# Optimization experiments

Hardware: AMD Instinct MI355X
Metric: run time of the kernel (lower is better)

The kernel has to match this reference:

```python
import jax, jax.numpy as jnp
import numpy as np

N, F = 12288, 512
NEG_INF = jnp.float32(-1e9)  # matches Keras BaseDenseAttention mask additive constant


def setup_inputs() -> dict:
    key = jax.random.key(0)
    k1, k2 = jax.random.split(key)
    features = jax.random.normal(k1, (N, F), dtype=jnp.float32)
    A = jax.random.randint(k2, (N, N), 0, 2).astype(jnp.int32)
    return {"features": features, "A": A}


def reference(features, A):
    # Keras Attention with query=key=value=dropout(features); dropout is identity
    # at inference. use_scale=False -> plain dot-product scores, no 1/sqrt(d).
    scores = jnp.einsum("nf,mf->nm", features, features)          # [N, N]
    scores = jnp.where(A > 0, scores, NEG_INF)                    # mask non-edges
    attn = jax.nn.softmax(scores, axis=-1)                        # softmax over keys
    return jnp.einsum("nm,mf->nf", attn, features)                # [N, F]
```

## Files before the change

kernel.cpp:

```cpp
#include <hip/hip_runtime.h>
#include <cstddef>
#include <cstdint>

#define NN 12288
#define FF 512

using half8 = __attribute__((ext_vector_type(8))) _Float16;
using half4 = __attribute__((ext_vector_type(4))) _Float16;
using f32x4 = __attribute__((ext_vector_type(4))) float;

constexpr float MASK_NEG = -1e9f;

__device__ __forceinline__ void gll16(const void* g, void* l) {
    __builtin_amdgcn_global_load_lds((const __attribute__((address_space(1))) void*)g,
                                     (__attribute__((address_space(3))) void*)l, 16, 0, 0);
}

__global__ void cvt_feat_kernel(const float* __restrict__ in, _Float16* __restrict__ out) {
    const size_t i = ((size_t)blockIdx.x * blockDim.x + threadIdx.x) * 8;
    float4 x = *reinterpret_cast<const float4*>(in + i);
    float4 y = *reinterpret_cast<const float4*>(in + i + 4);
    half8 h;
    h[0] = (_Float16)x.x; h[1] = (_Float16)x.y; h[2] = (_Float16)x.z; h[3] = (_Float16)x.w;
    h[4] = (_Float16)y.x; h[5] = (_Float16)y.y; h[6] = (_Float16)y.z; h[7] = (_Float16)y.w;
    *reinterpret_cast<half8*>(out + i) = h;
}

__global__ void transpose_feat_kernel(const float* __restrict__ in, _Float16* __restrict__ outT) {
    __shared__ float tile[32][33];
    const int bi = blockIdx.x;
    const int bj = blockIdx.y;
    const int r  = threadIdx.x >> 3;
    const int c4 = (threadIdx.x & 7) << 2;
    float4 v = *reinterpret_cast<const float4*>(in + (size_t)(bi * 32 + r) * FF + bj * 32 + c4);
    tile[r][c4 + 0] = v.x; tile[r][c4 + 1] = v.y; tile[r][c4 + 2] = v.z; tile[r][c4 + 3] = v.w;
    __syncthreads();
    half4 h;
#pragma unroll
    for (int k = 0; k < 4; ++k) h[k] = (_Float16)tile[c4 + k][r];
    *reinterpret_cast<half4*>(outT + (size_t)(bj * 32 + r) * NN + bi * 32 + c4) = h;
}

__global__ __launch_bounds__(256)
void gemm1_exp(const _Float16* __restrict__ feath, const int* __restrict__ Amat,
               _Float16* __restrict__ Pmat, float* __restrict__ m_t) {
    __shared__ alignas(16) _Float16 As[2][128 * 32];
    __shared__ alignas(16) _Float16 Bs[2][128 * 32];
    __shared__ alignas(16) float rowmax2[128][2];

    const int tid = threadIdx.x, lane = tid & 63, wid = tid >> 6;
    const int g = lane >> 4, a = lane & 15;
    const int wr = wid >> 1, wc = wid & 1;
    const int row0 = blockIdx.x * 128, col0 = blockIdx.y * 128;

    f32x4 acc[4][4];
#pragma unroll
    for (int i = 0; i < 4; ++i)
#pragma unroll
        for (int j = 0; j < 4; ++j) acc[i][j] = f32x4{0.f, 0.f, 0.f, 0.f};

    const int lr = lane >> 2;
    const int li = (lane & 3) * 8;

    auto stage = [&](int buf, int t) {
#pragma unroll
        for (int c = 0; c < 2; ++c) {
            const int ch = wid * 2 + c;
            gll16(feath + (size_t)(row0 + ch * 16 + lr) * FF + t * 32 + li, &As[buf][ch * 512]);
            gll16(feath + (size_t)(col0 + ch * 16 + lr) * FF + t * 32 + li, &Bs[buf][ch * 512]);
        }
    };

    stage(0, 0);
    __syncthreads();
    int buf = 0;
    for (int t = 0; t < 16; ++t) {
        if (t + 1 < 16) stage(buf ^ 1, t + 1);
        half8 af[4], bf[4];
#pragma unroll
        for (int rf = 0; rf < 4; ++rf)
            af[rf] = *reinterpret_cast<const half8*>(&As[buf][(64 * wr + 16 * rf + a) * 32 + 8 * g]);
#pragma unroll
        for (int cf = 0; cf < 4; ++cf)
            bf[cf] = *reinterpret_cast<const half8*>(&Bs[buf][(64 * wc + 16 * cf + a) * 32 + 8 * g]);
#pragma unroll
        for (int rf = 0; rf < 4; ++rf)
#pragma unroll
            for (int cf = 0; cf < 4; ++cf)
                acc[rf][cf] = __builtin_amdgcn_mfma_f32_16x16x32_f16(af[rf], bf[cf], acc[rf][cf], 0, 0, 0);
        __syncthreads();
        buf ^= 1;
    }

#pragma unroll
    for (int rf = 0; rf < 4; ++rf) {
#pragma unroll
        for (int r = 0; r < 4; ++r) {
            const int grow = row0 + 64 * wr + 16 * rf + 4 * g + r;
#pragma unroll
            for (int cf = 0; cf < 4; ++cf) {
                const int gcol = col0 + 64 * wc + 16 * cf + a;
                const int am = Amat[(size_t)grow * NN + gcol];
                acc[rf][cf][r] = (am > 0) ? acc[rf][cf][r] : MASK_NEG;
            }
        }
    }
#pragma unroll
    for (int rf = 0; rf < 4; ++rf) {
#pragma unroll
        for (int r = 0; r < 4; ++r) {
            float v = fmaxf(fmaxf(acc[rf][0][r], acc[rf][1][r]), fmaxf(acc[rf][2][r], acc[rf][3][r]));
            v = fmaxf(v, __shfl_xor(v, 1, 16));
            v = fmaxf(v, __shfl_xor(v, 2, 16));
            v = fmaxf(v, __shfl_xor(v, 4, 16));
            v = fmaxf(v, __shfl_xor(v, 8, 16));
            if (a == 0) rowmax2[64 * wr + 16 * rf + 4 * g + r][wc] = v;
        }
    }
    __syncthreads();
    if (tid < 128)
        m_t[(size_t)blockIdx.y * NN + row0 + tid] = fmaxf(rowmax2[tid][0], rowmax2[tid][1]);
#pragma unroll
    for (int rf = 0; rf < 4; ++rf) {
#pragma unroll
        for (int r = 0; r < 4; ++r) {
            const int lrow = 64 * wr + 16 * rf + 4 * g + r;
            const float mt = fmaxf(rowmax2[lrow][0], rowmax2[lrow][1]);
            const size_t rbase = (size_t)(row0 + lrow) * NN + col0 + 64 * wc + a;
#pragma unroll
            for (int cf = 0; cf < 4; ++cf) {
                const float p = __expf(acc[rf][cf][r] - mt);
                Pmat[rbase + 16 * cf] = (_Float16)p;
            }
        }
    }
}

__global__ __launch_bounds__(256)
void row_stats_kernel(const _Float16* __restrict__ Pmat, const float* __restrict__ m_t,
                      float* __restrict__ m_row, float* __restrict__ l_row) {
    const int lane = threadIdx.x & 63;
    const int wid  = threadIdx.x >> 6;
    const int row  = blockIdx.x * 4 + wid;

    float v = -3.0e38f;
    for (int kt = lane; kt < 96; kt += 64) v = fmaxf(v, m_t[(size_t)kt * NN + row]);
    v = fmaxf(v, __shfl_xor(v, 1));
    v = fmaxf(v, __shfl_xor(v, 2));
    v = fmaxf(v, __shfl_xor(v, 4));
    v = fmaxf(v, __shfl_xor(v, 8));
    v = fmaxf(v, __shfl_xor(v, 16));
    v = fmaxf(v, __shfl_xor(v, 32));
    const float m = v;

    float l = 0.f;
    const _Float16* prow = Pmat + (size_t)row * NN;
#pragma unroll 2
    for (int it = 0; it < 24; ++it) {
        half8 p = *reinterpret_cast<const half8*>(prow + it * 512 + lane * 8);
        float s = 0.f;
#pragma unroll
        for (int j = 0; j < 8; ++j) s += (float)p[j];
        s += __shfl_xor(s, 1, 16);
        s += __shfl_xor(s, 2, 16);
        s += __shfl_xor(s, 4, 16);
        s += __shfl_xor(s, 8, 16);
        const int kt = it * 4 + (lane >> 4);
        l += __expf(m_t[(size_t)kt * NN + row] - m) * s;
    }
    l += __shfl_xor(l, 16);
    l += __shfl_xor(l, 32);
    if (lane == 0) { m_row[row] = m; l_row[row] = l; }
}

__global__ __launch_bounds__(256)
void gemm2_scale(const _Float16* __restrict__ Pmat, const _Float16* __restrict__ featT,
                 const float* __restrict__ m_t, const float* __restrict__ m_row,
                 const float* __restrict__ l_row, float* __restrict__ out) {
    __shared__ alignas(16) _Float16 As[2][128 * 32];
    __shared__ alignas(16) _Float16 Bs[2][64 * 32];

    const int tid = threadIdx.x, lane = tid & 63, wid = tid >> 6;
    const int g = lane >> 4, a = lane & 15;
    const int wr = wid >> 1, wc = wid & 1;
    const int row0 = blockIdx.x * 128, col0 = blockIdx.y * 64;

    f32x4 acc[4][2];
#pragma unroll
    for (int i = 0; i < 4; ++i) { acc[i][0] = f32x4{0.f,0.f,0.f,0.f}; acc[i][1] = f32x4{0.f,0.f,0.f,0.f}; }

    float m_r[4];
#pragma unroll
    for (int rf = 0; rf < 4; ++rf) m_r[rf] = m_row[row0 + 64 * wr + 16 * rf + a];

    const int lr = lane >> 2;
    const int li = (lane & 3) * 8;

    auto stage = [&](int buf, int t) {
#pragma unroll
        for (int c = 0; c < 2; ++c) {
            const int ch = wid * 2 + c;
            gll16(Pmat + (size_t)(row0 + ch * 16 + lr) * NN + t * 32 + li, &As[buf][ch * 512]);
        }
        gll16(featT + (size_t)(col0 + wid * 16 + lr) * NN + t * 32 + li, &Bs[buf][wid * 512]);
    };

    stage(0, 0);
    __syncthreads();
    int buf = 0;
    _Float16 sc[4] = {(_Float16)1.f, (_Float16)1.f, (_Float16)1.f, (_Float16)1.f};
    for (int t = 0; t < 384; ++t) {
        if ((t & 3) == 0) {
            const int kt = t >> 2;
#pragma unroll
            for (int rf = 0; rf < 4; ++rf)
                sc[rf] = (_Float16)__expf(m_t[(size_t)kt * NN + row0 + 64 * wr + 16 * rf + a] - m_r[rf]);
        }
        if (t + 1 < 384) stage(buf ^ 1, t + 1);
        half8 af[4], bf[2];
#pragma unroll
        for (int rf = 0; rf < 4; ++rf) {
            af[rf] = *reinterpret_cast<const half8*>(&As[buf][(64 * wr + 16 * rf + a) * 32 + 8 * g]);
            af[rf] = af[rf] * sc[rf];
        }
#pragma unroll
        for (int cf = 0; cf < 2; ++cf)
            bf[cf] = *reinterpret_cast<const half8*>(&Bs[buf][(32 * wc + 16 * cf + a) * 32 + 8 * g]);
#pragma unroll
        for (int rf = 0; rf < 4; ++rf)
#pragma unroll
            for (int cf = 0; cf < 2; ++cf)
                acc[rf][cf] = __builtin_amdgcn_mfma_f32_16x16x32_f16(af[rf], bf[cf], acc[rf][cf], 0, 0, 0);
        __syncthreads();
        buf ^= 1;
    }

#pragma unroll
    for (int rf = 0; rf < 4; ++rf) {
#pragma unroll
        for (int r = 0; r < 4; ++r) {
            const int grow = row0 + 64 * wr + 16 * rf + 4 * g + r;
            const float il = 1.0f / l_row[grow];
#pragma unroll
            for (int cf = 0; cf < 2; ++cf) {
                const int gcol = col0 + 32 * wc + 16 * cf + a;
                out[(size_t)grow * FF + gcol] = acc[rf][cf][r] * il;
            }
        }
    }
}

constexpr int BM_ = 64;
constexpr int BN_ = 64;
constexpr int KV_STRIDE = 520;

template<bool RH>
__global__ __launch_bounds__(512, 2)
void attn_flash(const float* __restrict__ featf, const _Float16* __restrict__ feath,
                const int* __restrict__ Amat, float* __restrict__ out) {
    __shared__ alignas(16) _Float16 kv[BN_ * KV_STRIDE];
    __shared__ alignas(16) _Float16 pbuf[BM_][72];
    __shared__ alignas(16) float pmax[BM_][2];
    __shared__ alignas(16) float psum[BM_][2];
    __shared__ alignas(16) float m_s[BM_];
    __shared__ alignas(16) float l_s[BM_];
    __shared__ alignas(16) float rscale[BM_];

    const int tid  = threadIdx.x;
    const int lane = tid & 63;
    const int wid  = tid >> 6;
    const int g    = lane >> 4;
    const int a    = lane & 15;
    const int rg   = wid >> 1;
    const int ch   = wid & 1;
    const int qrow0 = blockIdx.x * BM_;

    half8 qf[16];
    {
        const int qr = qrow0 + 16 * rg + a;
#pragma unroll
        for (int ks = 0; ks < 16; ++ks) {
            const int f0 = 32 * ks + 8 * g;
            if constexpr (RH) {
                qf[ks] = *reinterpret_cast<const half8*>(feath + (size_t)qr * FF + f0);
            } else {
                const float* sp = featf + (size_t)qr * FF + f0;
                float4 x = *reinterpret_cast<const float4*>(sp);
                float4 y = *reinterpret_cast<const float4*>(sp + 4);
                half8 h;
                h[0] = (_Float16)x.x; h[1] = (_Float16)x.y; h[2] = (_Float16)x.z; h[3] = (_Float16)x.w;
                h[4] = (_Float16)y.x; h[5] = (_Float16)y.y; h[6] = (_Float16)y.z; h[7] = (_Float16)y.w;
                qf[ks] = h;
            }
        }
    }

    f32x4 acc[4][4];
#pragma unroll
    for (int i = 0; i < 4; ++i)
#pragma unroll
        for (int j = 0; j < 4; ++j) acc[i][j] = f32x4{0.f, 0.f, 0.f, 0.f};

    if (tid < BM_) { m_s[tid] = -INFINITY; l_s[tid] = 0.f; }
    __syncthreads();

    for (int kt = 0; kt < NN / BN_; ++kt) {
        const int key0 = kt * BN_;
#pragma unroll
        for (int i = 0; i < 8; ++i) {
            const int flat8 = tid + i * 512;
            const int key   = flat8 >> 6;
            const int b     = flat8 & 63;
            const int slot  = (b + (key >> 3)) & 63;
            _Float16* dst = &kv[key * KV_STRIDE + slot * 8];
            if constexpr (RH) {
                *reinterpret_cast<half8*>(dst) =
                    *reinterpret_cast<const half8*>(feath + (size_t)(key0 + key) * FF + b * 8);
            } else {
                const float* sp = featf + (size_t)(key0 + key) * FF + b * 8;
                float4 x = *reinterpret_cast<const float4*>(sp);
                float4 y = *reinterpret_cast<const float4*>(sp + 4);
                half8 h;
                h[0] = (_Float16)x.x; h[1] = (_Float16)x.y; h[2] = (_Float16)x.z; h[3] = (_Float16)x.w;
                h[4] = (_Float16)y.x; h[5] = (_Float16)y.y; h[6] = (_Float16)y.z; h[7] = (_Float16)y.w;
                *reinterpret_cast<half8*>(dst) = h;
            }
        }

        int am[2][4];
#pragma unroll
        for (int fc = 0; fc < 2; ++fc)
#pragma unroll
            for (int r = 0; r < 4; ++r) {
                const int arow = qrow0 + 16 * rg + 4 * g + r;
                const int acol = key0 + 32 * ch + 16 * fc + a;
                am[fc][r] = Amat[(size_t)arow * NN + acol];
            }
        __syncthreads();

        f32x4 s0{0.f, 0.f, 0.f, 0.f}, s1{0.f, 0.f, 0.f, 0.f};
        const int bk0 = 32 * ch + a;
        const int bk1 = bk0 + 16;
        const int kb0 = bk0 >> 3;
        const int kb1 = bk1 >> 3;
        const _Float16* kr0 = &kv[bk0 * KV_STRIDE];
        const _Float16* kr1 = &kv[bk1 * KV_STRIDE];
#pragma unroll
        for (int ks = 0; ks < 16; ++ks) {
            const int b = 4 * ks + g;
            const half8 bf0 = *reinterpret_cast<const half8*>(kr0 + (((b + kb0) & 63) << 3));
            const half8 bf1 = *reinterpret_cast<const half8*>(kr1 + (((b + kb1) & 63) << 3));
            s0 = __builtin_amdgcn_mfma_f32_16x16x32_f16(qf[ks], bf0, s0, 0, 0, 0);
            s1 = __builtin_amdgcn_mfma_f32_16x16x32_f16(qf[ks], bf1, s1, 0, 0, 0);
        }

        float sv[2][4];
#pragma unroll
        for (int r = 0; r < 4; ++r) {
            sv[0][r] = (am[0][r] > 0) ? s0[r] : MASK_NEG;
            sv[1][r] = (am[1][r] > 0) ? s1[r] : MASK_NEG;
        }
#pragma unroll
        for (int r = 0; r < 4; ++r) {
            float v = fmaxf(sv[0][r], sv[1][r]);
            v = fmaxf(v, __shfl_xor(v, 1, 16));
            v = fmaxf(v, __shfl_xor(v, 2, 16));
            v = fmaxf(v, __shfl_xor(v, 4, 16));
            v = fmaxf(v, __shfl_xor(v, 8, 16));
            if (a == 0) pmax[16 * rg + 4 * g + r][ch] = v;
        }
        __syncthreads();

#pragma unroll
        for (int r = 0; r < 4; ++r) {
            const int row = 16 * rg + 4 * g + r;
            const float mo = m_s[row];
            const float mn = fmaxf(mo, fmaxf(pmax[row][0], pmax[row][1]));
            const float p0 = __expf(sv[0][r] - mn);
            const float p1 = __expf(sv[1][r] - mn);
            pbuf[row][32 * ch + a]      = (_Float16)p0;
            pbuf[row][32 * ch + 16 + a] = (_Float16)p1;
            float ssum = p0 + p1;
            ssum += __shfl_xor(ssum, 1, 16);
            ssum += __shfl_xor(ssum, 2, 16);
            ssum += __shfl_xor(ssum, 4, 16);
            ssum += __shfl_xor(ssum, 8, 16);
            if (a == 0) psum[row][ch] = ssum;
        }
        __syncthreads();

        if (tid < BM_) {
            const float mo = m_s[tid];
            const float mn = fmaxf(mo, fmaxf(pmax[tid][0], pmax[tid][1]));
            const float sc = __expf(mo - mn);
            l_s[tid] = l_s[tid] * sc + psum[tid][0] + psum[tid][1];
            m_s[tid] = mn;
            rscale[tid] = sc;
        }
        __syncthreads();

#pragma unroll
        for (int rf = 0; rf < 4; ++rf) {
            const float4 scv = *reinterpret_cast<const float4*>(&rscale[16 * rf + 4 * g]);
#pragma unroll
            for (int cf = 0; cf < 4; ++cf) {
                acc[rf][cf][0] *= scv.x; acc[rf][cf][1] *= scv.y;
                acc[rf][cf][2] *= scv.z; acc[rf][cf][3] *= scv.w;
            }
        }
#pragma unroll
        for (int kk = 0; kk < 2; ++kk) {
            half8 af[4];
#pragma unroll
            for (int rf = 0; rf < 4; ++rf)
                af[rf] = *reinterpret_cast<const half8*>(&pbuf[16 * rf + a][32 * kk + 8 * g]);
            const int keybase = 32 * kk + 8 * g;
#pragma unroll
            for (int cf = 0; cf < 4; ++cf) {
                const int col  = 64 * wid + 16 * cf + a;
                const int slot = (((col >> 3) + 4 * kk + g) & 63);
                const _Float16* vb = &kv[(size_t)keybase * KV_STRIDE + (slot << 3) + (col & 7)];
                half8 bf;
#pragma unroll
                for (int j = 0; j < 8; ++j)
                    bf[j] = vb[j * KV_STRIDE];
#pragma unroll
                for (int rf = 0; rf < 4; ++rf)
                    acc[rf][cf] = __builtin_amdgcn_mfma_f32_16x16x32_f16(af[rf], bf, acc[rf][cf], 0, 0, 0);
            }
        }
        __syncthreads();
    }

#pragma unroll
    for (int rf = 0; rf < 4; ++rf) {
        const float4 lv = *reinterpret_cast<const float4*>(&l_s[16 * rf + 4 * g]);
        const float inv[4] = {1.f / lv.x, 1.f / lv.y, 1.f / lv.z, 1.f / lv.w};
#pragma unroll
        for (int cf = 0; cf < 4; ++cf) {
            const int col = 64 * wid + 16 * cf + a;
#pragma unroll
            for (int r = 0; r < 4; ++r) {
                out[(size_t)(qrow0 + 16 * rf + 4 * g + r) * FF + col] = acc[rf][cf][r] * inv[r];
            }
        }
    }
}

extern "C" void kernel_launch(void* const* d_in, const int* in_sizes, int n_in,
                              void* d_out, int out_size, void* d_ws, size_t ws_size,
                              hipStream_t stream) {
    const float* features = (const float*)d_in[0];
    const int*   Amat     = (const int*)d_in[1];
    float*       out      = (float*)d_out;

    const size_t P_bytes   = (size_t)NN * NN * 2;
    const size_t f16_bytes = (size_t)NN * FF * 2;
    const size_t mt_bytes  = (size_t)96 * NN * 4;
    const size_t mrow_b    = (size_t)NN * 4;
    const size_t total     = P_bytes + 2 * f16_bytes + mt_bytes + 2 * mrow_b;

    if (ws_size >= total) {
        char* w = (char*)d_ws;
        _Float16* Pmat  = (_Float16*)w;                       w += P_bytes;
        _Float16* feath = (_Float16*)w;                       w += f16_bytes;
        _Float16* featT = (_Float16*)w;                       w += f16_bytes;
        float*    m_t   = (float*)w;                          w += mt_bytes;
        float*    m_row = (float*)w;                          w += mrow_b;
        float*    l_row = (float*)w;

        cvt_feat_kernel<<<(NN * FF) / (256 * 8), 256, 0, stream>>>(features, feath);
        transpose_feat_kernel<<<dim3(NN / 32, FF / 32), 256, 0, stream>>>(features, featT);
        gemm1_exp<<<dim3(NN / 128, NN / 128), 256, 0, stream>>>(feath, Amat, Pmat, m_t);
        row_stats_kernel<<<NN / 4, 256, 0, stream>>>(Pmat, m_t, m_row, l_row);
        gemm2_scale<<<dim3(NN / 128, FF / 64), 256, 0, stream>>>(Pmat, featT, m_t, m_row, l_row, out);
    } else if (ws_size >= f16_bytes) {
        _Float16* feath = (_Float16*)d_ws;
        cvt_feat_kernel<<<(NN * FF) / (256 * 8), 256, 0, stream>>>(features, feath);
        attn_flash<true><<<NN / BM_, 512, 0, stream>>>(features, feath, Amat, out);
    } else {
        attn_flash<false><<<NN / BM_, 512, 0, stream>>>(features, nullptr, Amat, out);
    }
}
```

Before: 772.1 us.

## Bit-pack mask, fuse row-sum into GEMM1, precompute scales, widen GEMM2 tiles

A new pre-pass packs the int32 adjacency into bitmasks, which GEMM1 then reads instead of the full ints. GEMM1 now also emits per-tile partial row sums of the exponentials. That removes the separate pass that re-read the whole fp16 P matrix to compute row normalizers. A small stats kernel combines the per-tile max and sum and precomputes the fp16 rescale factors that GEMM2 loads instead of evaluating exponentials. GEMM2 switches to 128x128 tiles with a grid order that favours L2 reuse of P rows. The packed mask and tile maxima are staged in the output buffer as scratch, and the tile sums are kept in fp16, which costs some precision.

```diff
diff --git a/kernel.cpp b/kernel.cpp
--- a/kernel.cpp
+++ b/kernel.cpp
@@ -4,6 +4,8 @@
 
 #define NN 12288
 #define FF 512
+#define NWORDS (NN / 32)
+#define NKT (NN / 128)
 
 using half8 = __attribute__((ext_vector_type(8))) _Float16;
 using half4 = __attribute__((ext_vector_type(4))) _Float16;
@@ -14,6 +16,22 @@
 __device__ __forceinline__ void gll16(const void* g, void* l) {
     __builtin_amdgcn_global_load_lds((const __attribute__((address_space(1))) void*)g,
                                      (__attribute__((address_space(3))) void*)l, 16, 0, 0);
+}
+
+__global__ __launch_bounds__(256)
+void compress_mask_kernel(const int* __restrict__ Amat, uint32_t* __restrict__ Abits) {
+    const size_t W = (size_t)blockIdx.x * blockDim.x + threadIdx.x;
+    const int4* p = reinterpret_cast<const int4*>(Amat + W * 32);
+    uint32_t b = 0;
+#pragma unroll
+    for (int q = 0; q < 8; ++q) {
+        const int4 v = p[q];
+        b |= (uint32_t)(v.x > 0) << (4 * q + 0);
+        b |= (uint32_t)(v.y > 0) << (4 * q + 1);
+        b |= (uint32_t)(v.z > 0) << (4 * q + 2);
+        b |= (uint32_t)(v.w > 0) << (4 * q + 3);
+    }
+    Abits[W] = b;
 }
 
 __global__ void cvt_feat_kernel(const float* __restrict__ in, _Float16* __restrict__ out) {
@@ -42,11 +60,12 @@
 }
 
 __global__ __launch_bounds__(256)
-void gemm1_exp(const _Float16* __restrict__ feath, const int* __restrict__ Amat,
-               _Float16* __restrict__ Pmat, float* __restrict__ m_t) {
+void gemm1_exp(const _Float16* __restrict__ feath, const uint32_t* __restrict__ Abits,
+               _Float16* __restrict__ Pmat, float* __restrict__ m_t, _Float16* __restrict__ s_t) {
     __shared__ alignas(16) _Float16 As[2][128 * 32];
     __shared__ alignas(16) _Float16 Bs[2][128 * 32];
     __shared__ alignas(16) float rowmax2[128][2];
+    __shared__ alignas(16) float rowsum2[128][2];
 
     const int tid = threadIdx.x, lane = tid & 63, wid = tid >> 6;
     const int g = lane >> 4, a = lane & 15;
@@ -92,19 +111,27 @@
         buf ^= 1;
     }
 
-#pragma unroll
-    for (int rf = 0; rf < 4; ++rf) {
+    const int cw0 = (col0 + 64 * wc) >> 5;
+    uint2 am[4][4];
+#pragma unroll
+    for (int rf = 0; rf < 4; ++rf)
 #pragma unroll
         for (int r = 0; r < 4; ++r) {
             const int grow = row0 + 64 * wr + 16 * rf + 4 * g + r;
+            am[rf][r] = *reinterpret_cast<const uint2*>(&Abits[(size_t)grow * NWORDS + cw0]);
+        }
+#pragma unroll
+    for (int rf = 0; rf < 4; ++rf)
+#pragma unroll
+        for (int r = 0; r < 4; ++r) {
 #pragma unroll
             for (int cf = 0; cf < 4; ++cf) {
-                const int gcol = col0 + 64 * wc + 16 * cf + a;
-                const int am = Amat[(size_t)grow * NN + gcol];
-                acc[rf][cf][r] = (am > 0) ? acc[rf][cf][r] : MASK_NEG;
-            }
-        }
-    }
+                const uint32_t w = (cf < 2) ? am[rf][r].x : am[rf][r].y;
+                const uint32_t bit = (w >> (a + 16 * (cf & 1))) & 1u;
+                acc[rf][cf][r] = bit ? acc[rf][cf][r] : MASK_NEG;
+            }
+        }
+
 #pragma unroll
     for (int rf = 0; rf < 4; ++rf) {
 #pragma unroll
@@ -118,8 +145,7 @@
         }
     }
     __syncthreads();
-    if (tid < 128)
-        m_t[(size_t)blockIdx.y * NN + row0 + tid] = fmaxf(rowmax2[tid][0], rowmax2[tid][1]);
+
 #pragma unroll
     for (int rf = 0; rf < 4; ++rf) {
 #pragma unroll
@@ -127,71 +153,61 @@
             const int lrow = 64 * wr + 16 * rf + 4 * g + r;
             const float mt = fmaxf(rowmax2[lrow][0], rowmax2[lrow][1]);
             const size_t rbase = (size_t)(row0 + lrow) * NN + col0 + 64 * wc + a;
+            float ps = 0.f;
 #pragma unroll
             for (int cf = 0; cf < 4; ++cf) {
                 const float p = __expf(acc[rf][cf][r] - mt);
+                ps += p;
                 Pmat[rbase + 16 * cf] = (_Float16)p;
             }
-        }
+            ps += __shfl_xor(ps, 1, 16);
+            ps += __shfl_xor(ps, 2, 16);
+            ps += __shfl_xor(ps, 4, 16);
+            ps += __shfl_xor(ps, 8, 16);
+            if (a == 0) rowsum2[lrow][wc] = ps;
+        }
+    }
+    __syncthreads();
+    if (tid < 128) {
+        m_t[(size_t)blockIdx.y * NN + row0 + tid] = fmaxf(rowmax2[tid][0], rowmax2[tid][1]);
+        s_t[(size_t)blockIdx.y * NN + row0 + tid] = (_Float16)(rowsum2[tid][0] + rowsum2[tid][1]);
     }
 }
 
 __global__ __launch_bounds__(256)
-void row_stats_kernel(const _Float16* __restrict__ Pmat, const float* __restrict__ m_t,
-                      float* __restrict__ m_row, float* __restrict__ l_row) {
-    const int lane = threadIdx.x & 63;
-    const int wid  = threadIdx.x >> 6;
-    const int row  = blockIdx.x * 4 + wid;
-
-    float v = -3.0e38f;
-    for (int kt = lane; kt < 96; kt += 64) v = fmaxf(v, m_t[(size_t)kt * NN + row]);
-    v = fmaxf(v, __shfl_xor(v, 1));
-    v = fmaxf(v, __shfl_xor(v, 2));
-    v = fmaxf(v, __shfl_xor(v, 4));
-    v = fmaxf(v, __shfl_xor(v, 8));
-    v = fmaxf(v, __shfl_xor(v, 16));
-    v = fmaxf(v, __shfl_xor(v, 32));
-    const float m = v;
-
+void stats_kernel(const float* __restrict__ m_t, const _Float16* __restrict__ s_t,
+                  _Float16* __restrict__ sc_t, float* __restrict__ l_row) {
+    const int r = blockIdx.x * 256 + threadIdx.x;
+    float m = -3.0e38f;
+#pragma unroll 4
+    for (int kt = 0; kt < NKT; ++kt) m = fmaxf(m, m_t[(size_t)kt * NN + r]);
     float l = 0.f;
-    const _Float16* prow = Pmat + (size_t)row * NN;
-#pragma unroll 2
-    for (int it = 0; it < 24; ++it) {
-        half8 p = *reinterpret_cast<const half8*>(prow + it * 512 + lane * 8);
-        float s = 0.f;
-#pragma unroll
-        for (int j = 0; j < 8; ++j) s += (float)p[j];
-        s += __shfl_xor(s, 1, 16);
-        s += __shfl_xor(s, 2, 16);
-        s += __shfl_xor(s, 4, 16);
-        s += __shfl_xor(s, 8, 16);
-        const int kt = it * 4 + (lane >> 4);
-        l += __expf(m_t[(size_t)kt * NN + row] - m) * s;
-    }
-    l += __shfl_xor(l, 16);
-    l += __shfl_xor(l, 32);
-    if (lane == 0) { m_row[row] = m; l_row[row] = l; }
+#pragma unroll 4
+    for (int kt = 0; kt < NKT; ++kt) {
+        const float e = __expf(m_t[(size_t)kt * NN + r] - m);
+        sc_t[(size_t)kt * NN + r] = (_Float16)e;
+        l += e * (float)s_t[(size_t)kt * NN + r];
+    }
+    l_row[r] = l;
 }
 
 __global__ __launch_bounds__(256)
 void gemm2_scale(const _Float16* __restrict__ Pmat, const _Float16* __restrict__ featT,
-                 const float* __restrict__ m_t, const float* __restrict__ m_row,
-                 const float* __restrict__ l_row, float* __restrict__ out) {
+                 const _Float16* __restrict__ sc_t, const float* __restrict__ l_row,
+                 float* __restrict__ out) {
     __shared__ alignas(16) _Float16 As[2][128 * 32];
-    __shared__ alignas(16) _Float16 Bs[2][64 * 32];
+    __shared__ alignas(16) _Float16 Bs[2][128 * 32];
 
     const int tid = threadIdx.x, lane = tid & 63, wid = tid >> 6;
     const int g = lane >> 4, a = lane & 15;
     const int wr = wid >> 1, wc = wid & 1;
-    const int row0 = blockIdx.x * 128, col0 = blockIdx.y * 64;
-
-    f32x4 acc[4][2];
-#pragma unroll
-    for (int i = 0; i < 4; ++i) { acc[i][0] = f32x4{0.f,0.f,0.f,0.f}; acc[i][1] = f32x4{0.f,0.f,0.f,0.f}; }
-
-    float m_r[4];
-#pragma unroll
-    for (int rf = 0; rf < 4; ++rf) m_r[rf] = m_row[row0 + 64 * wr + 16 * rf + a];
+    const int col0 = blockIdx.x * 128, row0 = blockIdx.y * 128;
+
+    f32x4 acc[4][4];
+#pragma unroll
+    for (int i = 0; i < 4; ++i)
+#pragma unroll
+        for (int j = 0; j < 4; ++j) acc[i][j] = f32x4{0.f, 0.f, 0.f, 0.f};
 
     const int lr = lane >> 2;
     const int li = (lane & 3) * 8;
@@ -200,9 +216,9 @@
 #pragma unroll
         for (int c = 0; c < 2; ++c) {
             const int ch = wid * 2 + c;
-            gll16(Pmat + (size_t)(row0 + ch * 16 + lr) * NN + t * 32 + li, &As[buf][ch * 512]);
-        }
-        gll16(featT + (size_t)(col0 + wid * 16 + lr) * NN + t * 32 + li, &Bs[buf][wid * 512]);
+            gll16(Pmat  + (size_t)(row0 + ch * 16 + lr) * NN + t * 32 + li, &As[buf][ch * 512]);
+            gll16(featT + (size_t)(col0 + ch * 16 + lr) * NN + t * 32 + li, &Bs[buf][ch * 512]);
+        }
     };
 
     stage(0, 0);
@@ -214,22 +230,22 @@
             const int kt = t >> 2;
 #pragma unroll
             for (int rf = 0; rf < 4; ++rf)
-                sc[rf] = (_Float16)__expf(m_t[(size_t)kt * NN + row0 + 64 * wr + 16 * rf + a] - m_r[rf]);
+                sc[rf] = sc_t[(size_t)kt * NN + row0 + 64 * wr + 16 * rf + a];
         }
         if (t + 1 < 384) stage(buf ^ 1, t + 1);
-        half8 af[4], bf[2];
+        half8 af[4], bf[4];
 #pragma unroll
         for (int rf = 0; rf < 4; ++rf) {
             af[rf] = *reinterpret_cast<const half8*>(&As[buf][(64 * wr + 16 * rf + a) * 32 + 8 * g]);
             af[rf] = af[rf] * sc[rf];
         }
 #pragma unroll
-        for (int cf = 0; cf < 2; ++cf)
-            bf[cf] = *reinterpret_cast<const half8*>(&Bs[buf][(32 * wc + 16 * cf + a) * 32 + 8 * g]);
+        for (int cf = 0; cf < 4; ++cf)
+            bf[cf] = *reinterpret_cast<const half8*>(&Bs[buf][(64 * wc + 16 * cf + a) * 32 + 8 * g]);
 #pragma unroll
         for (int rf = 0; rf < 4; ++rf)
 #pragma unroll
-            for (int cf = 0; cf < 2; ++cf)
+            for (int cf = 0; cf < 4; ++cf)
                 acc[rf][cf] = __builtin_amdgcn_mfma_f32_16x16x32_f16(af[rf], bf[cf], acc[rf][cf], 0, 0, 0);
         __syncthreads();
         buf ^= 1;
@@ -242,8 +258,8 @@
             const int grow = row0 + 64 * wr + 16 * rf + 4 * g + r;
             const float il = 1.0f / l_row[grow];
 #pragma unroll
-            for (int cf = 0; cf < 2; ++cf) {
-                const int gcol = col0 + 32 * wc + 16 * cf + a;
+            for (int cf = 0; cf < 4; ++cf) {
+                const int gcol = col0 + 64 * wc + 16 * cf + a;
                 out[(size_t)grow * FF + gcol] = acc[rf][cf][r] * il;
             }
         }
@@ -456,24 +472,29 @@
 
     const size_t P_bytes   = (size_t)NN * NN * 2;
     const size_t f16_bytes = (size_t)NN * FF * 2;
-    const size_t mt_bytes  = (size_t)96 * NN * 4;
-    const size_t mrow_b    = (size_t)NN * 4;
-    const size_t total     = P_bytes + 2 * f16_bytes + mt_bytes + 2 * mrow_b;
+    const size_t sct_bytes = (size_t)NKT * NN * 2;
+    const size_t st_bytes  = (size_t)NKT * NN * 2;
+    const size_t l_bytes   = (size_t)NN * 4;
+    const size_t total     = P_bytes + 2 * f16_bytes + sct_bytes + st_bytes + l_bytes;
 
     if (ws_size >= total) {
         char* w = (char*)d_ws;
-        _Float16* Pmat  = (_Float16*)w;                       w += P_bytes;
-        _Float16* feath = (_Float16*)w;                       w += f16_bytes;
-        _Float16* featT = (_Float16*)w;                       w += f16_bytes;
-        float*    m_t   = (float*)w;                          w += mt_bytes;
-        float*    m_row = (float*)w;                          w += mrow_b;
+        _Float16* Pmat  = (_Float16*)w;   w += P_bytes;
+        _Float16* feath = (_Float16*)w;   w += f16_bytes;
+        _Float16* featT = (_Float16*)w;   w += f16_bytes;
+        _Float16* sc_t  = (_Float16*)w;   w += sct_bytes;
+        _Float16* s_t   = (_Float16*)w;   w += st_bytes;
         float*    l_row = (float*)w;
 
+        uint32_t* Abits = (uint32_t*)d_out;
+        float*    m_t   = (float*)((char*)d_out + (size_t)NN * NWORDS * 4);
+
+        compress_mask_kernel<<<(NN * NWORDS) / 256, 256, 0, stream>>>(Amat, Abits);
         cvt_feat_kernel<<<(NN * FF) / (256 * 8), 256, 0, stream>>>(features, feath);
         transpose_feat_kernel<<<dim3(NN / 32, FF / 32), 256, 0, stream>>>(features, featT);
-        gemm1_exp<<<dim3(NN / 128, NN / 128), 256, 0, stream>>>(feath, Amat, Pmat, m_t);
-        row_stats_kernel<<<NN / 4, 256, 0, stream>>>(Pmat, m_t, m_row, l_row);
-        gemm2_scale<<<dim3(NN / 128, FF / 64), 256, 0, stream>>>(Pmat, featT, m_t, m_row, l_row, out);
+        gemm1_exp<<<dim3(NN / 128, NN / 128), 256, 0, stream>>>(feath, Abits, Pmat, m_t, s_t);
+        stats_kernel<<<NN / 256, 256, 0, stream>>>(m_t, s_t, sc_t, l_row);
+        gemm2_scale<<<dim3(FF / 128, NN / 128), 256, 0, stream>>>(Pmat, featT, sc_t, l_row, out);
     } else if (ws_size >= f16_bytes) {
         _Float16* feath = (_Float16*)d_ws;
         cvt_feat_kernel<<<(NN * FF) / (256 * 8), 256, 0, stream>>>(features, feath);
```

After: 894.4 us. 1.16x slower.
